# Kernel optimization log

Hardware: AMD Instinct MI355X
Metric: run time of the kernel (lower is better)

The kernel has to match this reference:

```python
import jax, jax.numpy as jnp
import numpy as np
import math

D_MODEL = 1024
NUM_HEADS = 16
SEQ = 2048
BATCH = 2


def setup_inputs() -> dict:
    key = jax.random.key(0)
    ks = jax.random.split(key, 12)
    s = 1.0 / math.sqrt(D_MODEL)
    inp = {
        "query": jax.random.normal(ks[0], (SEQ, BATCH, D_MODEL), jnp.float32),
        "key": jax.random.normal(ks[1], (SEQ, BATCH, D_MODEL), jnp.float32),
        "value": jax.random.normal(ks[2], (SEQ, BATCH, D_MODEL), jnp.float32),
        "Wq": jax.random.normal(ks[3], (D_MODEL, D_MODEL), jnp.float32) * s,
        "bq": jax.random.normal(ks[4], (D_MODEL,), jnp.float32) * 0.01,
        "Wk": jax.random.normal(ks[5], (D_MODEL, D_MODEL), jnp.float32) * s,
        "bk": jax.random.normal(ks[6], (D_MODEL,), jnp.float32) * 0.01,
        "Wv": jax.random.normal(ks[7], (D_MODEL, D_MODEL), jnp.float32) * s,
        "bv": jax.random.normal(ks[8], (D_MODEL,), jnp.float32) * 0.01,
        "Wo": jax.random.normal(ks[9], (D_MODEL, D_MODEL), jnp.float32) * s,
        "bo": jax.random.normal(ks[10], (D_MODEL,), jnp.float32) * 0.01,
    }
    # causal (subsequent) mask: True above the diagonal means masked
    inp["attn_mask"] = jnp.triu(jnp.ones((SEQ, SEQ), bool), k=1)
    # key_padding_mask: True = padding; random lengths in [SEQ//2, SEQ]
    lengths = jax.random.randint(ks[11], (BATCH,), SEQ // 2, SEQ + 1)
    inp["key_padding_mask"] = jnp.arange(SEQ)[None, :] >= lengths[:, None]
    return inp


def reference(query, key, value, Wq, bq, Wk, bk, Wv, bv, Wo, bo, attn_mask, key_padding_mask):
    S, B, D = query.shape
    H = NUM_HEADS
    dk = D // H

    def proj_split(x, W, b):
        y = x @ W.T + b                      # [S, B, D]
        return y.reshape(S, B, H, dk).transpose(1, 2, 0, 3)  # [B, H, S, dk]

    q = proj_split(query, Wq, bq)
    k = proj_split(key, Wk, bk)
    v = proj_split(value, Wv, bv)

    scores = jnp.einsum("bhqd,bhkd->bhqk", q, k) / jnp.sqrt(jnp.float32(dk))
    mask = key_padding_mask[:, None, None, :] | attn_mask[None, None, :, :]
    scores = jnp.where(mask, -jnp.inf, scores)
    p = jax.nn.softmax(scores, axis=-1)       # [B, H, S, S]
    x = jnp.einsum("bhqk,bhkd->bhqd", p, v)   # [B, H, S, dk]
    x = x.transpose(2, 0, 1, 3).reshape(S, B, D)
    return x @ Wo.T + bo
```

## Files before the change

kernel.cpp:

```cpp
#include <hip/hip_runtime.h>
#include <hip/hip_bf16.h>

#define S_LEN 2048
#define BATCH 2
#define DMODEL 1024
#define NHEAD 16
#define DK 64

typedef __bf16 bf16_t;
typedef bf16_t bf16x4 __attribute__((ext_vector_type(4)));
typedef bf16_t bf16x8 __attribute__((ext_vector_type(8)));
typedef float floatx4 __attribute__((ext_vector_type(4)));

#define SEG  ((size_t)S_LEN * BATCH * DMODEL)
#define WSEG ((size_t)DMODEL * DMODEL)
#define CVT_TOT (3 * SEG + 4 * WSEG)

#define QSCALE 0.180336879f

__global__ void prep_lens(const unsigned char* __restrict__ am,
                          const unsigned char* __restrict__ kpm,
                          int* __restrict__ lens)
{
    __shared__ int stride_s;
    __shared__ int cnt[BATCH];
    const int t = threadIdx.x;
    if (t == 0) {
        int st;
        if (am[1]) st = 1;
        else if (am[2] | am[3]) st = 2;
        else st = 4;
        stride_s = st;
    }
    if (t < BATCH) cnt[t] = 0;
    __syncthreads();
    const int st = stride_s;
    for (int idx = t; idx < BATCH * S_LEN; idx += blockDim.x) {
        int nz = 0;
        for (int c = 0; c < st; c++) nz |= kpm[idx * st + c];
        if (nz) atomicAdd(&cnt[idx / S_LEN], 1);
    }
    __syncthreads();
    if (t < BATCH) lens[t] = S_LEN - cnt[t];
}

__global__ void cvt_all(const float* __restrict__ q, const float* __restrict__ k,
                        const float* __restrict__ v, const float* __restrict__ wq,
                        const float* __restrict__ wk, const float* __restrict__ wv,
                        const float* __restrict__ wo, bf16_t* __restrict__ out)
{
    size_t i4 = ((size_t)blockIdx.x * blockDim.x + threadIdx.x) * 4;
    const size_t stride = (size_t)gridDim.x * blockDim.x * 4;
    for (; i4 < CVT_TOT; i4 += stride) {
        const float* src;
        size_t off;
        if (i4 < SEG)                    { src = q;  off = i4; }
        else if (i4 < 2 * SEG)           { src = k;  off = i4 - SEG; }
        else if (i4 < 3 * SEG)           { src = v;  off = i4 - 2 * SEG; }
        else if (i4 < 3 * SEG + WSEG)    { src = wq; off = i4 - 3 * SEG; }
        else if (i4 < 3 * SEG + 2 * WSEG){ src = wk; off = i4 - (3 * SEG + WSEG); }
        else if (i4 < 3 * SEG + 3 * WSEG){ src = wv; off = i4 - (3 * SEG + 2 * WSEG); }
        else                             { src = wo; off = i4 - (3 * SEG + 3 * WSEG); }
        const float4 x = *(const float4*)(src + off);
        bf16x4 r;
        r[0] = (bf16_t)x.x; r[1] = (bf16_t)x.y; r[2] = (bf16_t)x.z; r[3] = (bf16_t)x.w;
        *(bf16x4*)(out + i4) = r;
    }
}

__global__ __launch_bounds__(256, 2)
void gemm_qkv(const bf16_t* __restrict__ Abase, const bf16_t* __restrict__ Wbase,
              const float* __restrict__ bq, const float* __restrict__ bk,
              const float* __restrict__ bv, bf16_t* __restrict__ Obase)
{
    __shared__ bf16_t As[128 * 32];
    __shared__ bf16_t Bs[128 * 32];

    const int z = blockIdx.z;
    const bf16_t* A = Abase + (size_t)z * SEG;
    const bf16_t* W = Wbase + (size_t)z * WSEG;
    const float* bias = (z == 0) ? bq : (z == 1) ? bk : bv;
    bf16_t* C = Obase + (size_t)z * SEG;

    const int t    = threadIdx.x;
    const int wave = t >> 6;
    const int lane = t & 63;
    const int l15  = lane & 15;
    const int quad = lane >> 4;

    const int mBase = blockIdx.y * 128;
    const int nBase = blockIdx.x * 128;
    const int wRow  = (wave >> 1) * 64;
    const int wCol  = (wave & 1) * 64;

    floatx4 acc[4][4];
#pragma unroll
    for (int i = 0; i < 4; i++)
#pragma unroll
        for (int j = 0; j < 4; j++) acc[i][j] = (floatx4){0.f, 0.f, 0.f, 0.f};

    for (int k0 = 0; k0 < DMODEL; k0 += 32) {
#pragma unroll
        for (int c = 0; c < 2; c++) {
            const int chunk = c * 256 + t;
            const int row   = chunk >> 2;
            const int col   = (chunk & 3) * 8;
            const bf16_t* gA = A + (size_t)(mBase + row) * DMODEL + k0 + col;
            const bf16_t* gB = W + (size_t)(nBase + row) * DMODEL + k0 + col;
            bf16_t* lA = As + (c * 256 + wave * 64) * 8;
            bf16_t* lB = Bs + (c * 256 + wave * 64) * 8;
            __builtin_amdgcn_global_load_lds(
                (const __attribute__((address_space(1))) void*)gA,
                (__attribute__((address_space(3))) void*)lA, 16, 0, 0);
            __builtin_amdgcn_global_load_lds(
                (const __attribute__((address_space(1))) void*)gB,
                (__attribute__((address_space(3))) void*)lB, 16, 0, 0);
        }
        __syncthreads();

        bf16x8 af[4], bfr[4];
#pragma unroll
        for (int mi = 0; mi < 4; mi++)
            af[mi] = *(const bf16x8*)(As + (wRow + mi * 16 + l15) * 32 + quad * 8);
#pragma unroll
        for (int ni = 0; ni < 4; ni++)
            bfr[ni] = *(const bf16x8*)(Bs + (wCol + ni * 16 + l15) * 32 + quad * 8);
#pragma unroll
        for (int mi = 0; mi < 4; mi++)
#pragma unroll
            for (int ni = 0; ni < 4; ni++)
                acc[mi][ni] = __builtin_amdgcn_mfma_f32_16x16x32_bf16(
                    af[mi], bfr[ni], acc[mi][ni], 0, 0, 0);
        __syncthreads();
    }

    const float scale = (z == 0) ? QSCALE : 1.0f;
    float bvv[4];
#pragma unroll
    for (int ni = 0; ni < 4; ni++)
        bvv[ni] = bias[nBase + wCol + ni * 16 + l15];

#pragma unroll
    for (int mi = 0; mi < 4; mi++) {
#pragma unroll
        for (int ni = 0; ni < 4; ni++) {
            const int n = nBase + wCol + ni * 16 + l15;
            const int h = n >> 6, i = n & 63;
#pragma unroll
            for (int j = 0; j < 4; j++) {
                const int m = mBase + wRow + mi * 16 + quad * 4 + j;
                const int s = m >> 1, b = m & 1;
                const float v = (acc[mi][ni][j] + bvv[ni]) * scale;
                size_t off;
                if (z < 2)
                    off = ((size_t)(b * NHEAD + h) * S_LEN + s) * DK + i;
                else
                    off = ((size_t)(b * NHEAD + h) * DK + i) * S_LEN + s;
                C[off] = (bf16_t)v;
            }
        }
    }
}

__global__ __launch_bounds__(256, 3)
void attn(const bf16_t* __restrict__ qw, const bf16_t* __restrict__ kw,
          const bf16_t* __restrict__ vw, bf16_t* __restrict__ ow,
          const int* __restrict__ lens)
{
    __shared__ bf16_t Ks[2][64 * 64];
    __shared__ bf16_t Vs[2][64 * 64];
    __shared__ bf16_t Ps[4][16 * 72];

    const int t    = threadIdx.x;
    const int wave = t >> 6;
    const int lane = t & 63;
    const int l15  = lane & 15;
    const int quad = lane >> 4;
    const int qg   = lane & 48;
    const int rowbase = qg >> 2;

    const int n     = (int)(blockIdx.x + (blockIdx.y << 5));
    const int bh    = (n & 7) | ((n >> 8) << 3);
    const int qTile = (((n >> 3) & 31) + ((n >> 8) << 3)) & 31;
    const int b     = bh >> 4;
    const int len   = lens[b];
    const int qBase = qTile * 64;

    const bf16_t* kbase = kw + (size_t)bh * S_LEN * DK;
    const bf16_t* vbase = vw + (size_t)bh * DK * S_LEN;

    const int dr = lane >> 3;
    const int cc = (lane & 7) ^ dr;

    const bf16_t* Qg = qw + ((size_t)bh * S_LEN + qBase + wave * 16) * DK;
    const bf16x8 qa0 = *(const bf16x8*)(Qg + l15 * DK + quad * 8);
    const bf16x8 qa1 = *(const bf16x8*)(Qg + l15 * DK + 32 + quad * 8);

    floatx4 O[4];
#pragma unroll
    for (int i = 0; i < 4; i++) O[i] = (floatx4){0.f, 0.f, 0.f, 0.f};
    float lrow = 0.f;

    const int ktEnd = min(qTile, (len - 1) >> 6);

    auto dma_tile = [&](int ktB, int buf) {
#pragma unroll
        for (int i = 0; i < 2; i++) {
            const int R0 = (wave * 2 + i) * 8;
            const bf16_t* gK = kbase + (size_t)(ktB + R0 + dr) * DK + cc * 8;
            const bf16_t* gV = vbase + (size_t)(R0 + dr) * S_LEN + ktB + cc * 8;
            bf16_t* lK = &Ks[buf][(size_t)R0 * 64];
            bf16_t* lV = &Vs[buf][(size_t)R0 * 64];
            __builtin_amdgcn_global_load_lds(
                (const __attribute__((address_space(1))) void*)gK,
                (__attribute__((address_space(3))) void*)lK, 16, 0, 0);
            __builtin_amdgcn_global_load_lds(
                (const __attribute__((address_space(1))) void*)gV,
                (__attribute__((address_space(3))) void*)lV, 16, 0, 0);
        }
    };

    dma_tile(0, 0);
    __syncthreads();

    const int sw  = l15 & 7;
    const int ch0 = (quad ^ sw) * 8;
    const int ch1 = ((4 | quad) ^ sw) * 8;

    for (int kt = 0; kt <= ktEnd; kt++) {
        const int cur = kt & 1;
        if (kt < ktEnd) dma_tile((kt + 1) * 64, cur ^ 1);

        floatx4 sc[4];
#pragma unroll
        for (int ni = 0; ni < 4; ni++) {
            const bf16_t* kr = &Ks[cur][(ni * 16 + l15) * 64];
            const bf16x8 kf0 = *(const bf16x8*)(kr + ch0);
            const bf16x8 kf1 = *(const bf16x8*)(kr + ch1);
            floatx4 zz = (floatx4){0.f, 0.f, 0.f, 0.f};
            zz = __builtin_amdgcn_mfma_f32_16x16x32_bf16(kf0, qa0, zz, 0, 0, 0);
            zz = __builtin_amdgcn_mfma_f32_16x16x32_bf16(kf1, qa1, zz, 0, 0, 0);
            sc[ni] = zz;
        }

        const int ktBase = kt * 64;
        const int q = qBase + wave * 16 + l15;
        const bool needMask = (kt == qTile) || (ktBase + 64 > len);
        if (needMask) {
#pragma unroll
            for (int ni = 0; ni < 4; ni++) {
#pragma unroll
                for (int r = 0; r < 4; r++) {
                    const int key = ktBase + ni * 16 + quad * 4 + r;
                    if (key > q || key >= len) sc[ni][r] = -3.0e38f;
                }
            }
        }

        float lsum = 0.f;
#pragma unroll
        for (int ni = 0; ni < 4; ni++) {
#pragma unroll
            for (int r = 0; r < 4; r++) {
                const float p = exp2f(sc[ni][r]);
                sc[ni][r] = p;
                lsum += p;
            }
        }
        lrow += lsum;

        bf16_t* Pw = Ps[wave];
#pragma unroll
        for (int ni = 0; ni < 4; ni++) {
            bf16x4 pk;
            pk[0] = (bf16_t)sc[ni][0]; pk[1] = (bf16_t)sc[ni][1];
            pk[2] = (bf16_t)sc[ni][2]; pk[3] = (bf16_t)sc[ni][3];
            *(bf16x4*)(Pw + l15 * 72 + ni * 16 + quad * 4) = pk;
        }

        const bf16x8 pa0 = *(const bf16x8*)(Pw + l15 * 72 + quad * 8);
        const bf16x8 pa1 = *(const bf16x8*)(Pw + l15 * 72 + 32 + quad * 8);
#pragma unroll
        for (int nd = 0; nd < 4; nd++) {
            const bf16_t* vr = &Vs[cur][(nd * 16 + l15) * 64];
            const bf16x8 vb0 = *(const bf16x8*)(vr + ch0);
            const bf16x8 vb1 = *(const bf16x8*)(vr + ch1);
            O[nd] = __builtin_amdgcn_mfma_f32_16x16x32_bf16(pa0, vb0, O[nd], 0, 0, 0);
            O[nd] = __builtin_amdgcn_mfma_f32_16x16x32_bf16(pa1, vb1, O[nd], 0, 0, 0);
        }
        __syncthreads();
    }

    lrow += __shfl_xor(lrow, 16);
    lrow += __shfl_xor(lrow, 32);

    float rinv[4];
#pragma unroll
    for (int j = 0; j < 4; j++)
        rinv[j] = 1.0f / __shfl(lrow, qg | (rowbase + j));
#pragma unroll
    for (int nd = 0; nd < 4; nd++) {
        const int d = (bh & 15) * DK + nd * 16 + l15;
#pragma unroll
        for (int j = 0; j < 4; j++) {
            const int qq = qBase + wave * 16 + quad * 4 + j;
            ow[((size_t)qq * BATCH + b) * DMODEL + d] = (bf16_t)(O[nd][j] * rinv[j]);
        }
    }
}

__global__ __launch_bounds__(256, 2)
void gemm_o(const bf16_t* __restrict__ A, const bf16_t* __restrict__ W,
            const float* __restrict__ bias, float* __restrict__ C)
{
    __shared__ bf16_t As[128 * 32];
    __shared__ bf16_t Bs[64 * 32];

    const int t    = threadIdx.x;
    const int wave = t >> 6;
    const int lane = t & 63;
    const int l15  = lane & 15;
    const int quad = lane >> 4;

    const int mBase = blockIdx.y * 128;
    const int nBase = blockIdx.x * 64;
    const int wRow  = wave * 32;

    floatx4 acc[2][4];
#pragma unroll
    for (int i = 0; i < 2; i++)
#pragma unroll
        for (int j = 0; j < 4; j++) acc[i][j] = (floatx4){0.f, 0.f, 0.f, 0.f};

    for (int k0 = 0; k0 < DMODEL; k0 += 32) {
#pragma unroll
        for (int c = 0; c < 2; c++) {
            const int chunk = c * 256 + t;
            const int row   = chunk >> 2;
            const int col   = (chunk & 3) * 8;
            const bf16_t* gA = A + (size_t)(mBase + row) * DMODEL + k0 + col;
            bf16_t* lA = As + (c * 256 + wave * 64) * 8;
            __builtin_amdgcn_global_load_lds(
                (const __attribute__((address_space(1))) void*)gA,
                (__attribute__((address_space(3))) void*)lA, 16, 0, 0);
        }
        {
            const int row = t >> 2;
            const int col = (t & 3) * 8;
            const bf16_t* gB = W + (size_t)(nBase + row) * DMODEL + k0 + col;
            bf16_t* lB = Bs + (wave * 64) * 8;
            __builtin_amdgcn_global_load_lds(
                (const __attribute__((address_space(1))) void*)gB,
                (__attribute__((address_space(3))) void*)lB, 16, 0, 0);
        }
        __syncthreads();

        bf16x8 af[2], bfr[4];
#pragma unroll
        for (int mi = 0; mi < 2; mi++)
            af[mi] = *(const bf16x8*)(As + (wRow + mi * 16 + l15) * 32 + quad * 8);
#pragma unroll
        for (int ni = 0; ni < 4; ni++)
            bfr[ni] = *(const bf16x8*)(Bs + (ni * 16 + l15) * 32 + quad * 8);
#pragma unroll
        for (int mi = 0; mi < 2; mi++)
#pragma unroll
            for (int ni = 0; ni < 4; ni++)
                acc[mi][ni] = __builtin_amdgcn_mfma_f32_16x16x32_bf16(
                    af[mi], bfr[ni], acc[mi][ni], 0, 0, 0);
        __syncthreads();
    }

    float bvv[4];
#pragma unroll
    for (int ni = 0; ni < 4; ni++)
        bvv[ni] = bias[nBase + ni * 16 + l15];

#pragma unroll
    for (int mi = 0; mi < 2; mi++) {
#pragma unroll
        for (int ni = 0; ni < 4; ni++) {
            const int n = nBase + ni * 16 + l15;
#pragma unroll
            for (int j = 0; j < 4; j++) {
                const int m = mBase + wRow + mi * 16 + quad * 4 + j;
                C[(size_t)m * DMODEL + n] = acc[mi][ni][j] + bvv[ni];
            }
        }
    }
}

extern "C" void kernel_launch(void* const* d_in, const int* in_sizes, int n_in,
                              void* d_out, int out_size, void* d_ws, size_t ws_size,
                              hipStream_t stream)
{
    const float* query = (const float*)d_in[0];
    const float* key   = (const float*)d_in[1];
    const float* value = (const float*)d_in[2];
    const float* Wq = (const float*)d_in[3];
    const float* bq = (const float*)d_in[4];
    const float* Wk = (const float*)d_in[5];
    const float* bk = (const float*)d_in[6];
    const float* Wv = (const float*)d_in[7];
    const float* bv = (const float*)d_in[8];
    const float* Wo = (const float*)d_in[9];
    const float* bo = (const float*)d_in[10];
    const unsigned char* am  = (const unsigned char*)d_in[11];
    const unsigned char* kpm = (const unsigned char*)d_in[12];

    bf16_t* cvt   = (bf16_t*)d_ws;
    bf16_t* q_bf  = cvt;
    bf16_t* wq_bf = cvt + 3 * SEG;
    bf16_t* wo_bf = wq_bf + 3 * WSEG;
    bf16_t* q_ws  = cvt + CVT_TOT;
    bf16_t* k_ws  = q_ws + SEG;
    bf16_t* v_ws  = k_ws + SEG;
    bf16_t* o_ws  = q_bf;
    int*    lens  = (int*)(v_ws + SEG);

    prep_lens<<<1, 256, 0, stream>>>(am, kpm, lens);
    cvt_all<<<4096, 256, 0, stream>>>(query, key, value, Wq, Wk, Wv, Wo, cvt);

    gemm_qkv<<<dim3(DMODEL / 128, (S_LEN * BATCH) / 128, 3), dim3(256), 0, stream>>>(
        q_bf, wq_bf, bq, bk, bv, q_ws);

    attn<<<dim3(32, BATCH * NHEAD), dim3(256), 0, stream>>>(
        q_ws, k_ws, v_ws, o_ws, lens);

    gemm_o<<<dim3(DMODEL / 64, (S_LEN * BATCH) / 128), dim3(256), 0, stream>>>(
        o_ws, wo_bf, bo, (float*)d_out);
}
```

Measured before the change: 251.5 us.

## Pair causal query tiles per block to balance work and share K/V loads

Each attention block now processes two query tiles, t and 31-t, so every block does roughly the same amount of causal work, and each K/V tile loaded into LDS is reused by both query tiles. The grid is halved and occupancy hint lowered from 3 to 2 blocks to fit doubled accumulators and registers. The P staging buffer row stride changes from 72 to 70 to alter LDS bank mapping. Costs: more registers per thread, fewer blocks in flight, and fewer total blocks (512) to fill the GPU.

```diff
diff --git a/kernel.cpp b/kernel.cpp
--- a/kernel.cpp
+++ b/kernel.cpp
@@ -162,14 +162,14 @@
     }
 }
 
-__global__ __launch_bounds__(256, 3)
+__global__ __launch_bounds__(256, 2)
 void attn(const bf16_t* __restrict__ qw, const bf16_t* __restrict__ kw,
           const bf16_t* __restrict__ vw, bf16_t* __restrict__ ow,
           const int* __restrict__ lens)
 {
     __shared__ bf16_t Ks[2][64 * 64];
     __shared__ bf16_t Vs[2][64 * 64];
-    __shared__ bf16_t Ps[4][16 * 72];
+    __shared__ bf16_t Ps[4][2][16 * 70];
 
     const int t    = threadIdx.x;
     const int wave = t >> 6;
@@ -179,12 +179,16 @@
     const int qg   = lane & 48;
     const int rowbase = qg >> 2;
 
-    const int n     = (int)(blockIdx.x + (blockIdx.y << 5));
-    const int bh    = (n & 7) | ((n >> 8) << 3);
-    const int qTile = (((n >> 3) & 31) + ((n >> 8) << 3)) & 31;
-    const int b     = bh >> 4;
-    const int len   = lens[b];
-    const int qBase = qTile * 64;
+    const int n    = (int)(blockIdx.x + (blockIdx.y << 4));
+    const int bh   = (n & 7) | ((n >> 7) << 3);
+    const int pair = (n >> 3) & 15;
+    const int b    = bh >> 4;
+    const int len  = lens[b];
+
+    const int tA = pair;
+    const int tB = 31 - pair;
+    const int qBaseA = tA * 64;
+    const int qBaseB = tB * 64;
 
     const bf16_t* kbase = kw + (size_t)bh * S_LEN * DK;
     const bf16_t* vbase = vw + (size_t)bh * DK * S_LEN;
@@ -192,16 +196,25 @@
     const int dr = lane >> 3;
     const int cc = (lane & 7) ^ dr;
 
-    const bf16_t* Qg = qw + ((size_t)bh * S_LEN + qBase + wave * 16) * DK;
-    const bf16x8 qa0 = *(const bf16x8*)(Qg + l15 * DK + quad * 8);
-    const bf16x8 qa1 = *(const bf16x8*)(Qg + l15 * DK + 32 + quad * 8);
-
-    floatx4 O[4];
-#pragma unroll
-    for (int i = 0; i < 4; i++) O[i] = (floatx4){0.f, 0.f, 0.f, 0.f};
-    float lrow = 0.f;
-
-    const int ktEnd = min(qTile, (len - 1) >> 6);
+    const bf16_t* QgA = qw + ((size_t)bh * S_LEN + qBaseA + wave * 16) * DK;
+    const bf16x8 qaA0 = *(const bf16x8*)(QgA + l15 * DK + quad * 8);
+    const bf16x8 qaA1 = *(const bf16x8*)(QgA + l15 * DK + 32 + quad * 8);
+    const bf16_t* QgB = qw + ((size_t)bh * S_LEN + qBaseB + wave * 16) * DK;
+    const bf16x8 qaB0 = *(const bf16x8*)(QgB + l15 * DK + quad * 8);
+    const bf16x8 qaB1 = *(const bf16x8*)(QgB + l15 * DK + 32 + quad * 8);
+
+    floatx4 OA[4], OB[4];
+#pragma unroll
+    for (int i = 0; i < 4; i++) {
+        OA[i] = (floatx4){0.f, 0.f, 0.f, 0.f};
+        OB[i] = (floatx4){0.f, 0.f, 0.f, 0.f};
+    }
+    float lrowA = 0.f, lrowB = 0.f;
+
+    const int lcap   = (len - 1) >> 6;
+    const int ktEndA = min(tA, lcap);
+    const int ktEndB = min(tB, lcap);
+    const int ktEnd  = (ktEndA > ktEndB) ? ktEndA : ktEndB;
 
     auto dma_tile = [&](int ktB, int buf) {
 #pragma unroll
@@ -227,10 +240,9 @@
     const int ch0 = (quad ^ sw) * 8;
     const int ch1 = ((4 | quad) ^ sw) * 8;
 
-    for (int kt = 0; kt <= ktEnd; kt++) {
-        const int cur = kt & 1;
-        if (kt < ktEnd) dma_tile((kt + 1) * 64, cur ^ 1);
-
+    auto tile_step = [&](int kt, int cur, int which,
+                         const bf16x8& a0, const bf16x8& a1,
+                         floatx4* O, float& lrow, int qTile, int qBase) {
         floatx4 sc[4];
 #pragma unroll
         for (int ni = 0; ni < 4; ni++) {
@@ -238,8 +250,8 @@
             const bf16x8 kf0 = *(const bf16x8*)(kr + ch0);
             const bf16x8 kf1 = *(const bf16x8*)(kr + ch1);
             floatx4 zz = (floatx4){0.f, 0.f, 0.f, 0.f};
-            zz = __builtin_amdgcn_mfma_f32_16x16x32_bf16(kf0, qa0, zz, 0, 0, 0);
-            zz = __builtin_amdgcn_mfma_f32_16x16x32_bf16(kf1, qa1, zz, 0, 0, 0);
+            zz = __builtin_amdgcn_mfma_f32_16x16x32_bf16(kf0, a0, zz, 0, 0, 0);
+            zz = __builtin_amdgcn_mfma_f32_16x16x32_bf16(kf1, a1, zz, 0, 0, 0);
             sc[ni] = zz;
         }
 
@@ -269,17 +281,17 @@
         }
         lrow += lsum;
 
-        bf16_t* Pw = Ps[wave];
+        bf16_t* Pw = Ps[wave][which];
 #pragma unroll
         for (int ni = 0; ni < 4; ni++) {
             bf16x4 pk;
             pk[0] = (bf16_t)sc[ni][0]; pk[1] = (bf16_t)sc[ni][1];
             pk[2] = (bf16_t)sc[ni][2]; pk[3] = (bf16_t)sc[ni][3];
-            *(bf16x4*)(Pw + l15 * 72 + ni * 16 + quad * 4) = pk;
-        }
-
-        const bf16x8 pa0 = *(const bf16x8*)(Pw + l15 * 72 + quad * 8);
-        const bf16x8 pa1 = *(const bf16x8*)(Pw + l15 * 72 + 32 + quad * 8);
+            *(bf16x4*)(Pw + l15 * 70 + ni * 16 + quad * 4) = pk;
+        }
+
+        const bf16x8 pa0 = *(const bf16x8*)(Pw + l15 * 70 + quad * 8);
+        const bf16x8 pa1 = *(const bf16x8*)(Pw + l15 * 70 + 32 + quad * 8);
 #pragma unroll
         for (int nd = 0; nd < 4; nd++) {
             const bf16_t* vr = &Vs[cur][(nd * 16 + l15) * 64];
@@ -288,25 +300,37 @@
             O[nd] = __builtin_amdgcn_mfma_f32_16x16x32_bf16(pa0, vb0, O[nd], 0, 0, 0);
             O[nd] = __builtin_amdgcn_mfma_f32_16x16x32_bf16(pa1, vb1, O[nd], 0, 0, 0);
         }
+    };
+
+    for (int kt = 0; kt <= ktEnd; kt++) {
+        const int cur = kt & 1;
+        if (kt < ktEnd) dma_tile((kt + 1) * 64, cur ^ 1);
+        if (kt <= ktEndA)
+            tile_step(kt, cur, 0, qaA0, qaA1, OA, lrowA, tA, qBaseA);
+        if (kt <= ktEndB)
+            tile_step(kt, cur, 1, qaB0, qaB1, OB, lrowB, tB, qBaseB);
         __syncthreads();
     }
 
-    lrow += __shfl_xor(lrow, 16);
-    lrow += __shfl_xor(lrow, 32);
-
-    float rinv[4];
-#pragma unroll
-    for (int j = 0; j < 4; j++)
-        rinv[j] = 1.0f / __shfl(lrow, qg | (rowbase + j));
-#pragma unroll
-    for (int nd = 0; nd < 4; nd++) {
-        const int d = (bh & 15) * DK + nd * 16 + l15;
-#pragma unroll
-        for (int j = 0; j < 4; j++) {
-            const int qq = qBase + wave * 16 + quad * 4 + j;
-            ow[((size_t)qq * BATCH + b) * DMODEL + d] = (bf16_t)(O[nd][j] * rinv[j]);
-        }
-    }
+    auto epilogue = [&](floatx4* O, float lrow, int qBase) {
+        lrow += __shfl_xor(lrow, 16);
+        lrow += __shfl_xor(lrow, 32);
+        float rinv[4];
+#pragma unroll
+        for (int j = 0; j < 4; j++)
+            rinv[j] = 1.0f / __shfl(lrow, qg | (rowbase + j));
+#pragma unroll
+        for (int nd = 0; nd < 4; nd++) {
+            const int d = (bh & 15) * DK + nd * 16 + l15;
+#pragma unroll
+            for (int j = 0; j < 4; j++) {
+                const int qq = qBase + wave * 16 + quad * 4 + j;
+                ow[((size_t)qq * BATCH + b) * DMODEL + d] = (bf16_t)(O[nd][j] * rinv[j]);
+            }
+        }
+    };
+    epilogue(OA, lrowA, qBaseA);
+    epilogue(OB, lrowB, qBaseB);
 }
 
 __global__ __launch_bounds__(256, 2)
@@ -424,7 +448,7 @@
     gemm_qkv<<<dim3(DMODEL / 128, (S_LEN * BATCH) / 128, 3), dim3(256), 0, stream>>>(
         q_bf, wq_bf, bq, bk, bv, q_ws);
 
-    attn<<<dim3(32, BATCH * NHEAD), dim3(256), 0, stream>>>(
+    attn<<<dim3(16, BATCH * NHEAD), dim3(256), 0, stream>>>(
         q_ws, k_ws, v_ws, o_ws, lens);
 
     gemm_o<<<dim3(DMODEL / 64, (S_LEN * BATCH) / 128), dim3(256), 0, stream>>>(
```

New measurement: 279.0 us. 10.9% more time.
